# Kernel tuning notes

Measured on AMD Instinct MI355X. Metric: run time of the kernel, lower is better.

The kernel has to match this reference:

```python
import jax, jax.numpy as jnp
import numpy as np

D_MODEL = 1024
NUM_HEADS = 16
THETA = 10000.0


def setup_inputs() -> dict:
    key = jax.random.key(0)
    ks = jax.random.split(key, 5)
    B, S, D = 4, 2048, D_MODEL
    std = float(np.sqrt(2.0 / (D + D)))
    x = jax.random.normal(ks[0], (B, S, D), dtype=jnp.float32)
    wq = jax.random.normal(ks[1], (D, D), dtype=jnp.float32) * std
    wk = jax.random.normal(ks[2], (D, D), dtype=jnp.float32) * std
    wv = jax.random.normal(ks[3], (D, D), dtype=jnp.float32) * std
    wo = jax.random.normal(ks[4], (D, D), dtype=jnp.float32) * std
    token_positions = jnp.broadcast_to(jnp.arange(S, dtype=jnp.int32), (B, S))
    return {"x": x, "token_positions": token_positions,
            "wq": wq, "wk": wk, "wv": wv, "wo": wo}


def _rope(t, token_positions, d_k):
    # t: [B, H, S, d_k]; token_positions: [B, S]
    freqs = 1.0 / (THETA ** (jnp.arange(0, d_k, 2, dtype=jnp.float32) / d_k))  # [d_k/2]
    angles = token_positions.astype(jnp.float32)[..., None] * freqs            # [B, S, d_k/2]
    angles = jnp.repeat(angles, 2, axis=-1)                                    # [B, S, d_k]
    cos = jnp.cos(angles)[:, None, :, :]  # broadcast over heads
    sin = jnp.sin(angles)[:, None, :, :]
    t1, t2 = t[..., 0::2], t[..., 1::2]
    t_rot = jnp.stack([-t2, t1], axis=-1).reshape(t.shape)  # interleave (-x2, x1)
    return t * cos + t_rot * sin


def reference(x, token_positions, wq, wk, wv, wo):
    B, S, D = x.shape
    H = NUM_HEADS
    d_k = D // H
    def proj(w):
        return (x @ w.T).reshape(B, S, H, d_k).transpose(0, 2, 1, 3)  # [B,H,S,dk]
    q = _rope(proj(wq), token_positions, d_k)
    k = _rope(proj(wk), token_positions, d_k)
    v = proj(wv)
    scale = 1.0 / jnp.sqrt(jnp.float32(d_k))
    scores = jnp.einsum('bhqd,bhkd->bhqk', q, k) * scale  # [B,H,S,S]
    causal = jnp.tril(jnp.ones((S, S), dtype=bool))
    scores = jnp.where(causal, scores, -jnp.inf)
    attn = jax.nn.softmax(scores, axis=-1)
    out = jnp.einsum('bhqk,bhkd->bhqd', attn, v)          # [B,H,S,dk]
    out = out.transpose(0, 2, 1, 3).reshape(B, S, D)
    return out @ wo.T
```

## Files before the change

### kernel.cpp

```cpp
#include <hip/hip_runtime.h>
#include <hip/hip_bf16.h>
#include <cstdint>
#include <cstddef>

#define B_ 4
#define S_ 2048
#define D_ 1024
#define H_ 16
#define DK_ 64
#define NTOK (B_*S_)

typedef __bf16 bf16;
typedef __bf16 bf16x8 __attribute__((ext_vector_type(8)));
typedef short s16x4 __attribute__((ext_vector_type(4)));
typedef float f32x4 __attribute__((ext_vector_type(4)));

#define AS1 __attribute__((address_space(1)))
#define AS3 __attribute__((address_space(3)))

static __device__ __forceinline__ short f2bf_s(float f) {
    return __builtin_bit_cast(short, (__bf16)f);
}

static __device__ __forceinline__ f32x4 mfma16(s16x4 a, s16x4 b, f32x4 c) {
#if __has_builtin(__builtin_amdgcn_mfma_f32_16x16x16bf16_1k)
    return __builtin_amdgcn_mfma_f32_16x16x16bf16_1k(a, b, c, 0, 0, 0);
#else
    asm volatile("v_mfma_f32_16x16x16_bf16 %0, %1, %2, %0\n\ts_nop 7\n\ts_nop 7"
                 : "+v"(c) : "v"(a), "v"(b));
    return c;
#endif
}

__global__ void cvt_all(const float* __restrict__ x, const float* __restrict__ wq,
                        const float* __restrict__ wk, const float* __restrict__ wv,
                        const float* __restrict__ wo, bf16* __restrict__ dst) {
    const int NX8 = NTOK * D_ / 8;
    const int W8 = D_ * D_ / 8;
    int i = blockIdx.x * blockDim.x + threadIdx.x;
    if (i >= NX8 + 4 * W8) return;
    const float* src; int j;
    if (i < NX8) { src = x; j = i; }
    else {
        int k = i - NX8;
        int w = k >> 17;
        j = k & (W8 - 1);
        src = w == 0 ? wq : (w == 1 ? wk : (w == 2 ? wv : wo));
    }
    const float4* s4 = reinterpret_cast<const float4*>(src) + (size_t)j * 2;
    float4 a = s4[0], b = s4[1];
    bf16x8 o;
    o[0] = (bf16)a.x; o[1] = (bf16)a.y; o[2] = (bf16)a.z; o[3] = (bf16)a.w;
    o[4] = (bf16)b.x; o[5] = (bf16)b.y; o[6] = (bf16)b.z; o[7] = (bf16)b.w;
    reinterpret_cast<bf16x8*>(dst)[i] = o;
}

__global__ void rope_table(const int* __restrict__ pos, float2* __restrict__ tab) {
    int i = blockIdx.x * blockDim.x + threadIdx.x;
    if (i >= NTOK * 32) return;
    int n = i >> 5, p = i & 31;
    float pf = (float)pos[n];
    float freq = powf(10000.0f, -(float)p * (1.0f / 32.0f));
    float ang = pf * freq;
    float s, c;
    sincosf(ang, &s, &c);
    tab[i] = make_float2(c, s);
}

__global__ __launch_bounds__(256, 2)
void gemm_qkv(const bf16* __restrict__ A, const bf16* __restrict__ Bw,
              bf16* __restrict__ Qr, bf16* __restrict__ Kz, bf16* __restrict__ VT,
              const float2* __restrict__ tab) {
    const float SCL2E = 0.125f * 1.44269504088896340736f;
    constexpr int NKT = 16;
    __shared__ alignas(16) bf16 lds[2][(128 + 128) * 64];
    const int tid = threadIdx.x;
    const int lane = tid & 63;
    const int wid = tid >> 6;
    const int wm = wid >> 1, wn = wid & 1;
    const int lr = lane & 15, lg = lane >> 4;
    const int m0 = blockIdx.x * 128;
    const int n0g = blockIdx.y * 128;

    f32x4 acc[4][4] = {};

    auto stage = [&](int kt, int bufi) {
        bf16* dst = &lds[bufi][0];
#pragma unroll
        for (int j = 0; j < 4; ++j) {
            int flat = j * 256 + tid;
            int r = flat >> 3, c = flat & 7;
            const bf16* src = A + (size_t)(m0 + r) * 1024 + kt * 64 + ((c ^ (r & 7)) << 3);
            __builtin_amdgcn_global_load_lds((const AS1 uint32_t*)src,
                                             (AS3 uint32_t*)(dst + (size_t)flat * 8), 16, 0, 0);
        }
#pragma unroll
        for (int j = 0; j < 4; ++j) {
            int flat = j * 256 + tid;
            int r = flat >> 3, c = flat & 7;
            const bf16* src = Bw + (size_t)(n0g + r) * 1024 + kt * 64 + ((c ^ (r & 7)) << 3);
            __builtin_amdgcn_global_load_lds((const AS1 uint32_t*)src,
                                             (AS3 uint32_t*)(dst + 128 * 64 + (size_t)flat * 8), 16, 0, 0);
        }
    };

    stage(0, 0);

    for (int kt = 0; kt < NKT; ++kt) {
        const bf16* bufA = &lds[kt & 1][0];
        const bf16* bufB = bufA + 128 * 64;

        asm volatile("" ::: "memory");
        __builtin_amdgcn_s_barrier();
        asm volatile("" ::: "memory");
        if (kt + 1 < NKT) {
            stage(kt + 1, (kt + 1) & 1);
            asm volatile("s_waitcnt vmcnt(8)" ::: "memory");
        } else {
            asm volatile("s_waitcnt vmcnt(0)" ::: "memory");
        }
        __builtin_amdgcn_s_barrier();
        asm volatile("" ::: "memory");

        const int sx = lr & 7;
        bf16x8 af[4][2], bfr[4][2];
#pragma unroll
        for (int mf = 0; mf < 4; ++mf)
#pragma unroll
            for (int kh = 0; kh < 2; ++kh)
                af[mf][kh] = *reinterpret_cast<const bf16x8*>(
                    &bufA[(wm * 64 + mf * 16 + lr) * 64 + (((kh * 4 + lg) ^ sx) << 3)]);
#pragma unroll
        for (int nf = 0; nf < 4; ++nf)
#pragma unroll
            for (int kh = 0; kh < 2; ++kh)
                bfr[nf][kh] = *reinterpret_cast<const bf16x8*>(
                    &bufB[(wn * 64 + nf * 16 + lr) * 64 + (((kh * 4 + lg) ^ sx) << 3)]);
        __builtin_amdgcn_s_setprio(1);
#pragma unroll
        for (int mf = 0; mf < 4; ++mf)
#pragma unroll
            for (int nf = 0; nf < 4; ++nf)
#pragma unroll
                for (int kh = 0; kh < 2; ++kh)
                    acc[mf][nf] = __builtin_amdgcn_mfma_f32_16x16x32_bf16(af[mf][kh], bfr[nf][kh], acc[mf][nf], 0, 0, 0);
        __builtin_amdgcn_s_setprio(0);
    }

#pragma unroll
    for (int mf = 0; mf < 4; ++mf) {
#pragma unroll
        for (int nf = 0; nf < 4; ++nf) {
            int row0 = m0 + wm * 64 + mf * 16 + lg * 4;
            int colg = n0g + wn * 64 + nf * 16 + lr;
            int which = colg >> 10;
            int col = colg & 1023;
            if (which < 2) {
#pragma unroll
                for (int r = 0; r < 4; ++r) {
                    int row = row0 + r;
                    float v = acc[mf][nf][r];
                    float partner = __shfl_xor(v, 1, 64);
                    float2 cs = tab[(size_t)row * 32 + ((col >> 1) & 31)];
                    float o = (col & 1) ? fmaf(v, cs.x, partner * cs.y)
                                        : fmaf(v, cs.x, -partner * cs.y);
                    if (which == 0) {
                        Qr[(size_t)row * 1024 + col] = (bf16)(o * SCL2E);
                    } else {
                        int h = col >> 6, e = col & 63;
                        int e2 = e ^ ((row & 7) << 3);
                        Kz[(size_t)row * 1024 + h * 64 + e2] = (bf16)o;
                    }
                }
            } else {
                int h = col >> 6, dd = col & 63;
                int kvb = row0 & 63;
                int sw = (((dd & 7) ^ ((dd >> 3) & 7)) & 7) << 3;
                s16x4 pk;
#pragma unroll
                for (int r = 0; r < 4; ++r) pk[r] = f2bf_s(acc[mf][nf][r]);
                size_t addr = ((((size_t)((row0 >> 11) * 16 + h)) * 32 + ((row0 >> 6) & 31)) * 64 + dd) * 64
                              + (size_t)(kvb ^ sw);
                *reinterpret_cast<s16x4*>(&VT[addr]) = pk;
            }
        }
    }
}

__global__ __launch_bounds__(256, 2)
void gemm_out(const bf16* __restrict__ A, const bf16* __restrict__ Bw,
              float* __restrict__ Cp) {
    constexpr int NKT = 16;
    __shared__ alignas(16) bf16 lds[2][(128 + 128) * 64];
    const int tid = threadIdx.x;
    const int lane = tid & 63;
    const int wid = tid >> 6;
    const int wm = wid >> 1, wn = wid & 1;
    const int lr = lane & 15, lg = lane >> 4;
    const int m0 = blockIdx.x * 128;
    const int n0g = blockIdx.y * 128;

    f32x4 acc[4][4] = {};

    auto stage = [&](int kt, int bufi) {
        bf16* dst = &lds[bufi][0];
#pragma unroll
        for (int j = 0; j < 4; ++j) {
            int flat = j * 256 + tid;
            int r = flat >> 3, c = flat & 7;
            const bf16* src = A + (size_t)(m0 + r) * 1024 + kt * 64 + ((c ^ (r & 7)) << 3);
            __builtin_amdgcn_global_load_lds((const AS1 uint32_t*)src,
                                             (AS3 uint32_t*)(dst + (size_t)flat * 8), 16, 0, 0);
        }
#pragma unroll
        for (int j = 0; j < 4; ++j) {
            int flat = j * 256 + tid;
            int r = flat >> 3, c = flat & 7;
            const bf16* src = Bw + (size_t)(n0g + r) * 1024 + kt * 64 + ((c ^ (r & 7)) << 3);
            __builtin_amdgcn_global_load_lds((const AS1 uint32_t*)src,
                                             (AS3 uint32_t*)(dst + 128 * 64 + (size_t)flat * 8), 16, 0, 0);
        }
    };

    stage(0, 0);

    for (int kt = 0; kt < NKT; ++kt) {
        const bf16* bufA = &lds[kt & 1][0];
        const bf16* bufB = bufA + 128 * 64;

        asm volatile("" ::: "memory");
        __builtin_amdgcn_s_barrier();
        asm volatile("" ::: "memory");
        if (kt + 1 < NKT) {
            stage(kt + 1, (kt + 1) & 1);
            asm volatile("s_waitcnt vmcnt(8)" ::: "memory");
        } else {
            asm volatile("s_waitcnt vmcnt(0)" ::: "memory");
        }
        __builtin_amdgcn_s_barrier();
        asm volatile("" ::: "memory");

        const int sx = lr & 7;
        bf16x8 af[4][2], bfr[4][2];
#pragma unroll
        for (int mf = 0; mf < 4; ++mf)
#pragma unroll
            for (int kh = 0; kh < 2; ++kh)
                af[mf][kh] = *reinterpret_cast<const bf16x8*>(
                    &bufA[(wm * 64 + mf * 16 + lr) * 64 + (((kh * 4 + lg) ^ sx) << 3)]);
#pragma unroll
        for (int nf = 0; nf < 4; ++nf)
#pragma unroll
            for (int kh = 0; kh < 2; ++kh)
                bfr[nf][kh] = *reinterpret_cast<const bf16x8*>(
                    &bufB[(wn * 64 + nf * 16 + lr) * 64 + (((kh * 4 + lg) ^ sx) << 3)]);
        __builtin_amdgcn_s_setprio(1);
#pragma unroll
        for (int mf = 0; mf < 4; ++mf)
#pragma unroll
            for (int nf = 0; nf < 4; ++nf)
#pragma unroll
                for (int kh = 0; kh < 2; ++kh)
                    acc[mf][nf] = __builtin_amdgcn_mfma_f32_16x16x32_bf16(af[mf][kh], bfr[nf][kh], acc[mf][nf], 0, 0, 0);
        __builtin_amdgcn_s_setprio(0);
    }

#pragma unroll
    for (int mf = 0; mf < 4; ++mf)
#pragma unroll
        for (int nf = 0; nf < 4; ++nf)
#pragma unroll
            for (int r = 0; r < 4; ++r) {
                int row = m0 + wm * 64 + mf * 16 + lg * 4 + r;
                int colg = n0g + wn * 64 + nf * 16 + lr;
                Cp[(size_t)row * 1024 + colg] = acc[mf][nf][r];
            }
}

__global__ __launch_bounds__(256, 2)
void flash_attn9(const bf16* __restrict__ Q, const bf16* __restrict__ Kz,
                 const bf16* __restrict__ VT, bf16* __restrict__ O) {
    __shared__ bf16 Ks[2][64 * 64];
    __shared__ bf16 Vt[2][64 * 64];
    const int tid = threadIdx.x, lane = tid & 63, w = tid >> 6;
    const int lr = lane & 15, lg = lane >> 4;
    const int qtA = blockIdx.x;
    const int qtB = 15 - qtA;
    const int q0[2] = { qtA * 128, qtB * 128 };
    const int ntS[2] = { 2 * qtA + 2, 2 * qtB + 2 };
    const int NT = ntS[1];
    const int bh = blockIdx.y;
    const int b = bh >> 4, h = bh & 15;
    const size_t base = ((size_t)b * S_) * D_ + (size_t)h * DK_;
    const size_t vtbase = (size_t)bh * 32 * 4096;

    bf16x8 aq[2][2][2];
#pragma unroll
    for (int si = 0; si < 2; ++si)
#pragma unroll
        for (int qs = 0; qs < 2; ++qs) {
            int qrow = q0[si] + w * 32 + qs * 16 + lr;
            const bf16* qp = Q + base + (size_t)qrow * D_ + lg * 8;
            aq[si][qs][0] = *reinterpret_cast<const bf16x8*>(qp);
            aq[si][qs][1] = *reinterpret_cast<const bf16x8*>(qp + 32);
        }

    f32x4 acc[2][2][4] = {};
    float m_run[2][2] = {{-1e30f, -1e30f}, {-1e30f, -1e30f}};
    float l_run[2][2] = {{0.f, 0.f}, {0.f, 0.f}};

    const int sjj = tid >> 3;
    const int se0 = (tid & 7) * 8;

    auto stage = [&](int t, int bufi) {
        bf16* kd = Ks[bufi];
        bf16* vd = Vt[bufi];
#pragma unroll
        for (int i = 0; i < 2; ++i) {
            int jj = sjj + i * 32;
            const bf16* ksrc = Kz + base + (size_t)(t * 64 + jj) * 1024 + se0;
            __builtin_amdgcn_global_load_lds((const AS1 uint32_t*)ksrc,
                                             (AS3 uint32_t*)(kd + jj * 64 + se0), 16, 0, 0);
            const bf16* vsrc = VT + vtbase + (size_t)t * 4096 + jj * 64 + se0;
            __builtin_amdgcn_global_load_lds((const AS1 uint32_t*)vsrc,
                                             (AS3 uint32_t*)(vd + jj * 64 + se0), 16, 0, 0);
        }
    };

    stage(0, 0);

    for (int t = 0; t < NT; ++t) {
        const int j0 = t * 64;
        const bf16* KsB = Ks[t & 1];
        const bf16* VtB = Vt[t & 1];

        asm volatile("" ::: "memory");
        __builtin_amdgcn_s_barrier();
        asm volatile("" ::: "memory");
        if (t + 1 < NT) {
            stage(t + 1, (t + 1) & 1);
            asm volatile("s_waitcnt vmcnt(4)" ::: "memory");
        } else {
            asm volatile("s_waitcnt vmcnt(0)" ::: "memory");
        }
        __builtin_amdgcn_s_barrier();
        asm volatile("" ::: "memory");

#pragma unroll
        for (int si = 0; si < 2; ++si) {
            if (t >= ntS[si]) continue;
            const int qmaxw = q0[si] + w * 32 + 31;
            if (j0 > qmaxw) continue;

            f32x4 sc[2][4];
            __builtin_amdgcn_s_setprio(1);
#pragma unroll
            for (int nt = 0; nt < 4; ++nt) {
                int krow = nt * 16 + lr;
                int swz = (krow & 7) << 3;
                bf16x8 a0 = *reinterpret_cast<const bf16x8*>(&KsB[krow * 64 + ((lg * 8) ^ swz)]);
                bf16x8 a1 = *reinterpret_cast<const bf16x8*>(&KsB[krow * 64 + ((32 + lg * 8) ^ swz)]);
#pragma unroll
                for (int qs = 0; qs < 2; ++qs) {
                    f32x4 tv = {};
                    tv = __builtin_amdgcn_mfma_f32_16x16x32_bf16(a0, aq[si][qs][0], tv, 0, 0, 0);
                    tv = __builtin_amdgcn_mfma_f32_16x16x32_bf16(a1, aq[si][qs][1], tv, 0, 0, 0);
                    sc[qs][nt] = tv;
                }
            }
            __builtin_amdgcn_s_setprio(0);

            s16x4 ap[2][4];
#pragma unroll
            for (int qs = 0; qs < 2; ++qs) {
                const int qrow = q0[si] + w * 32 + qs * 16 + lr;
                if (j0 + 63 > q0[si] + w * 32 + qs * 16) {
#pragma unroll
                    for (int nt = 0; nt < 4; ++nt)
#pragma unroll
                        for (int r = 0; r < 4; ++r) {
                            int kv = j0 + nt * 16 + lg * 4 + r;
                            if (kv > qrow) sc[qs][nt][r] = -1e30f;
                        }
                }
                float tmax = sc[qs][0][0];
#pragma unroll
                for (int nt = 0; nt < 4; ++nt)
#pragma unroll
                    for (int r = 0; r < 4; ++r) tmax = fmaxf(tmax, sc[qs][nt][r]);
                tmax = fmaxf(tmax, __shfl_xor(tmax, 16, 64));
                tmax = fmaxf(tmax, __shfl_xor(tmax, 32, 64));
                float mold = m_run[si][qs];
                if (!__all(tmax - mold <= 8.0f)) {
                    float mnew = fmaxf(mold, tmax);
                    float corr = exp2f(mold - mnew);
                    m_run[si][qs] = mnew;
                    l_run[si][qs] *= corr;
#pragma unroll
                    for (int r = 0; r < 4; ++r) {
                        float cr = __shfl(corr, (lane & 48) | (lg * 4 + r), 64);
#pragma unroll
                        for (int dt = 0; dt < 4; ++dt) acc[si][qs][dt][r] *= cr;
                    }
                }
                float mnow = m_run[si][qs];
                float rs = 0.f;
#pragma unroll
                for (int nt = 0; nt < 4; ++nt)
#pragma unroll
                    for (int r = 0; r < 4; ++r) {
                        float p = exp2f(sc[qs][nt][r] - mnow);
                        rs += p;
                        ap[qs][nt][r] = f2bf_s(p);
                    }
                rs += __shfl_xor(rs, 16, 64);
                rs += __shfl_xor(rs, 32, 64);
                l_run[si][qs] += rs;
            }

            __builtin_amdgcn_s_setprio(1);
#pragma unroll
            for (int dt = 0; dt < 4; ++dt) {
                int vrow = dt * 16 + lr;
                int vswz = (((vrow & 7) ^ (vrow >> 3)) & 7) << 3;
                s16x4 bv[4];
#pragma unroll
                for (int nt = 0; nt < 4; ++nt)
                    bv[nt] = *reinterpret_cast<const s16x4*>(&VtB[vrow * 64 + ((nt * 16 + lg * 4) ^ vswz)]);
#pragma unroll
                for (int qs = 0; qs < 2; ++qs)
#pragma unroll
                    for (int nt = 0; nt < 4; ++nt)
                        acc[si][qs][dt] = mfma16(ap[qs][nt], bv[nt], acc[si][qs][dt]);
            }
            __builtin_amdgcn_s_setprio(0);
        }
    }

#pragma unroll
    for (int si = 0; si < 2; ++si)
#pragma unroll
        for (int qs = 0; qs < 2; ++qs) {
            float inv = __builtin_amdgcn_rcpf(l_run[si][qs]);
#pragma unroll
            for (int r = 0; r < 4; ++r) {
                float invr = __shfl(inv, (lane & 48) | (lg * 4 + r), 64);
                int row = q0[si] + w * 32 + qs * 16 + lg * 4 + r;
#pragma unroll
                for (int dt = 0; dt < 4; ++dt)
                    O[base + (size_t)row * D_ + dt * 16 + lr] = (bf16)(acc[si][qs][dt][r] * invr);
            }
        }
}

extern "C" void kernel_launch(void* const* d_in, const int* in_sizes, int n_in,
                              void* d_out, int out_size, void* d_ws, size_t ws_size,
                              hipStream_t stream) {
    const float* x  = (const float*)d_in[0];
    const int*   tp = (const int*)d_in[1];
    const float* wq = (const float*)d_in[2];
    const float* wk = (const float*)d_in[3];
    const float* wv = (const float*)d_in[4];
    const float* wo = (const float*)d_in[5];

    bf16* ws = (bf16*)d_ws;
    bf16* Xbf = ws;
    bf16* Wqb = Xbf + (size_t)NTOK * D_;
    bf16* Wkb = Wqb + (size_t)D_ * D_;
    bf16* Wvb = Wkb + (size_t)D_ * D_;
    bf16* Wob = Wvb + (size_t)D_ * D_;
    bf16* Qr  = Wob + (size_t)D_ * D_;
    bf16* Kz  = Qr + (size_t)NTOK * D_;
    bf16* VT  = Kz + (size_t)NTOK * D_;
    bf16* AO  = VT + (size_t)NTOK * D_;
    float2* tab = (float2*)(AO + (size_t)NTOK * D_);
    (void)ws_size; (void)in_sizes; (void)n_in; (void)out_size;
    (void)Wkb; (void)Wvb;

    {
        int ntot8 = (NTOK * D_ + 4 * D_ * D_) / 8;
        cvt_all<<<(ntot8 + 255) / 256, 256, 0, stream>>>(x, wq, wk, wv, wo, Xbf);
    }
    rope_table<<<(NTOK * 32 + 255) / 256, 256, 0, stream>>>(tp, tab);

    gemm_qkv<<<dim3(NTOK / 128, 24), 256, 0, stream>>>(Xbf, Wqb, Qr, Kz, VT, tab);

    flash_attn9<<<dim3(8, B_ * H_), 256, 0, stream>>>(Qr, Kz, VT, AO);

    gemm_out<<<dim3(NTOK / 128, D_ / 128), 256, 0, stream>>>(AO, Wob, (float*)d_out);
}
```

Before: 214.0 us.

## Split GEMM B-tile prefetch mid-iteration and batch attention score MFMAs across strips

Result: no change. 211.9 us (-1.0%).

```diff
diff --git a/kernel.cpp b/kernel.cpp
--- a/kernel.cpp
+++ b/kernel.cpp
@@ -84,7 +84,7 @@
 
     f32x4 acc[4][4] = {};
 
-    auto stage = [&](int kt, int bufi) {
+    auto stageA = [&](int kt, int bufi) {
         bf16* dst = &lds[bufi][0];
 #pragma unroll
         for (int j = 0; j < 4; ++j) {
@@ -94,17 +94,21 @@
             __builtin_amdgcn_global_load_lds((const AS1 uint32_t*)src,
                                              (AS3 uint32_t*)(dst + (size_t)flat * 8), 16, 0, 0);
         }
+    };
+    auto stageB = [&](int kt, int bufi) {
+        bf16* dst = &lds[bufi][0] + 128 * 64;
 #pragma unroll
         for (int j = 0; j < 4; ++j) {
             int flat = j * 256 + tid;
             int r = flat >> 3, c = flat & 7;
             const bf16* src = Bw + (size_t)(n0g + r) * 1024 + kt * 64 + ((c ^ (r & 7)) << 3);
             __builtin_amdgcn_global_load_lds((const AS1 uint32_t*)src,
-                                             (AS3 uint32_t*)(dst + 128 * 64 + (size_t)flat * 8), 16, 0, 0);
+                                             (AS3 uint32_t*)(dst + (size_t)flat * 8), 16, 0, 0);
         }
     };
 
-    stage(0, 0);
+    stageA(0, 0);
+    stageB(0, 0);
 
     for (int kt = 0; kt < NKT; ++kt) {
         const bf16* bufA = &lds[kt & 1][0];
@@ -114,8 +118,8 @@
         __builtin_amdgcn_s_barrier();
         asm volatile("" ::: "memory");
         if (kt + 1 < NKT) {
-            stage(kt + 1, (kt + 1) & 1);
-            asm volatile("s_waitcnt vmcnt(8)" ::: "memory");
+            stageA(kt + 1, (kt + 1) & 1);
+            asm volatile("s_waitcnt vmcnt(4)" ::: "memory");
         } else {
             asm volatile("s_waitcnt vmcnt(0)" ::: "memory");
         }
@@ -131,7 +135,7 @@
                 af[mf][kh] = *reinterpret_cast<const bf16x8*>(
                     &bufA[(wm * 64 + mf * 16 + lr) * 64 + (((kh * 4 + lg) ^ sx) << 3)]);
 #pragma unroll
-        for (int nf = 0; nf < 4; ++nf)
+        for (int nf = 0; nf < 2; ++nf)
 #pragma unroll
             for (int kh = 0; kh < 2; ++kh)
                 bfr[nf][kh] = *reinterpret_cast<const bf16x8*>(
@@ -140,7 +144,26 @@
 #pragma unroll
         for (int mf = 0; mf < 4; ++mf)
 #pragma unroll
-            for (int nf = 0; nf < 4; ++nf)
+            for (int nf = 0; nf < 2; ++nf)
+#pragma unroll
+                for (int kh = 0; kh < 2; ++kh)
+                    acc[mf][nf] = __builtin_amdgcn_mfma_f32_16x16x32_bf16(af[mf][kh], bfr[nf][kh], acc[mf][nf], 0, 0, 0);
+        __builtin_amdgcn_s_setprio(0);
+        if (kt + 1 < NKT) stageB(kt + 1, (kt + 1) & 1);
+        asm volatile("" ::: "memory");
+        __builtin_amdgcn_s_barrier();
+        asm volatile("" ::: "memory");
+#pragma unroll
+        for (int nf = 2; nf < 4; ++nf)
+#pragma unroll
+            for (int kh = 0; kh < 2; ++kh)
+                bfr[nf][kh] = *reinterpret_cast<const bf16x8*>(
+                    &bufB[(wn * 64 + nf * 16 + lr) * 64 + (((kh * 4 + lg) ^ sx) << 3)]);
+        __builtin_amdgcn_s_setprio(1);
+#pragma unroll
+        for (int mf = 0; mf < 4; ++mf)
+#pragma unroll
+            for (int nf = 2; nf < 4; ++nf)
 #pragma unroll
                 for (int kh = 0; kh < 2; ++kh)
                     acc[mf][nf] = __builtin_amdgcn_mfma_f32_16x16x32_bf16(af[mf][kh], bfr[nf][kh], acc[mf][nf], 0, 0, 0);
@@ -202,7 +225,7 @@
 
     f32x4 acc[4][4] = {};
 
-    auto stage = [&](int kt, int bufi) {
+    auto stageA = [&](int kt, int bufi) {
         bf16* dst = &lds[bufi][0];
 #pragma unroll
         for (int j = 0; j < 4; ++j) {
@@ -212,17 +235,21 @@
             __builtin_amdgcn_global_load_lds((const AS1 uint32_t*)src,
                                              (AS3 uint32_t*)(dst + (size_t)flat * 8), 16, 0, 0);
         }
+    };
+    auto stageB = [&](int kt, int bufi) {
+        bf16* dst = &lds[bufi][0] + 128 * 64;
 #pragma unroll
         for (int j = 0; j < 4; ++j) {
             int flat = j * 256 + tid;
             int r = flat >> 3, c = flat & 7;
             const bf16* src = Bw + (size_t)(n0g + r) * 1024 + kt * 64 + ((c ^ (r & 7)) << 3);
             __builtin_amdgcn_global_load_lds((const AS1 uint32_t*)src,
-                                             (AS3 uint32_t*)(dst + 128 * 64 + (size_t)flat * 8), 16, 0, 0);
+                                             (AS3 uint32_t*)(dst + (size_t)flat * 8), 16, 0, 0);
         }
     };
 
-    stage(0, 0);
+    stageA(0, 0);
+    stageB(0, 0);
 
     for (int kt = 0; kt < NKT; ++kt) {
         const bf16* bufA = &lds[kt & 1][0];
@@ -232,8 +259,8 @@
         __builtin_amdgcn_s_barrier();
         asm volatile("" ::: "memory");
         if (kt + 1 < NKT) {
-            stage(kt + 1, (kt + 1) & 1);
-            asm volatile("s_waitcnt vmcnt(8)" ::: "memory");
+            stageA(kt + 1, (kt + 1) & 1);
+            asm volatile("s_waitcnt vmcnt(4)" ::: "memory");
         } else {
             asm volatile("s_waitcnt vmcnt(0)" ::: "memory");
         }
@@ -249,7 +276,7 @@
                 af[mf][kh] = *reinterpret_cast<const bf16x8*>(
                     &bufA[(wm * 64 + mf * 16 + lr) * 64 + (((kh * 4 + lg) ^ sx) << 3)]);
 #pragma unroll
-        for (int nf = 0; nf < 4; ++nf)
+        for (int nf = 0; nf < 2; ++nf)
 #pragma unroll
             for (int kh = 0; kh < 2; ++kh)
                 bfr[nf][kh] = *reinterpret_cast<const bf16x8*>(
@@ -258,7 +285,26 @@
 #pragma unroll
         for (int mf = 0; mf < 4; ++mf)
 #pragma unroll
-            for (int nf = 0; nf < 4; ++nf)
+            for (int nf = 0; nf < 2; ++nf)
+#pragma unroll
+                for (int kh = 0; kh < 2; ++kh)
+                    acc[mf][nf] = __builtin_amdgcn_mfma_f32_16x16x32_bf16(af[mf][kh], bfr[nf][kh], acc[mf][nf], 0, 0, 0);
+        __builtin_amdgcn_s_setprio(0);
+        if (kt + 1 < NKT) stageB(kt + 1, (kt + 1) & 1);
+        asm volatile("" ::: "memory");
+        __builtin_amdgcn_s_barrier();
+        asm volatile("" ::: "memory");
+#pragma unroll
+        for (int nf = 2; nf < 4; ++nf)
+#pragma unroll
+            for (int kh = 0; kh < 2; ++kh)
+                bfr[nf][kh] = *reinterpret_cast<const bf16x8*>(
+                    &bufB[(wn * 64 + nf * 16 + lr) * 64 + (((kh * 4 + lg) ^ sx) << 3)]);
+        __builtin_amdgcn_s_setprio(1);
+#pragma unroll
+        for (int mf = 0; mf < 4; ++mf)
+#pragma unroll
+            for (int nf = 2; nf < 4; ++nf)
 #pragma unroll
                 for (int kh = 0; kh < 2; ++kh)
                     acc[mf][nf] = __builtin_amdgcn_mfma_f32_16x16x32_bf16(af[mf][kh], bfr[nf][kh], acc[mf][nf], 0, 0, 0);
@@ -278,8 +324,8 @@
 }
 
 __global__ __launch_bounds__(256, 2)
-void flash_attn9(const bf16* __restrict__ Q, const bf16* __restrict__ Kz,
-                 const bf16* __restrict__ VT, bf16* __restrict__ O) {
+void flash_attn10(const bf16* __restrict__ Q, const bf16* __restrict__ Kz,
+                  const bf16* __restrict__ VT, bf16* __restrict__ O) {
     __shared__ bf16 Ks[2][64 * 64];
     __shared__ bf16 Vt[2][64 * 64];
     const int tid = threadIdx.x, lane = tid & 63, w = tid >> 6;
@@ -346,14 +392,14 @@
         __builtin_amdgcn_s_barrier();
         asm volatile("" ::: "memory");
 
+        const bool act[2] = { t < ntS[0] && j0 <= q0[0] + w * 32 + 31,
+                              j0 <= q0[1] + w * 32 + 31 };
+        f32x4 sc[2][2][4];
+
+        __builtin_amdgcn_s_setprio(1);
 #pragma unroll
         for (int si = 0; si < 2; ++si) {
-            if (t >= ntS[si]) continue;
-            const int qmaxw = q0[si] + w * 32 + 31;
-            if (j0 > qmaxw) continue;
-
-            f32x4 sc[2][4];
-            __builtin_amdgcn_s_setprio(1);
+            if (!act[si]) continue;
 #pragma unroll
             for (int nt = 0; nt < 4; ++nt) {
                 int krow = nt * 16 + lr;
@@ -365,10 +411,15 @@
                     f32x4 tv = {};
                     tv = __builtin_amdgcn_mfma_f32_16x16x32_bf16(a0, aq[si][qs][0], tv, 0, 0, 0);
                     tv = __builtin_amdgcn_mfma_f32_16x16x32_bf16(a1, aq[si][qs][1], tv, 0, 0, 0);
-                    sc[qs][nt] = tv;
+                    sc[si][qs][nt] = tv;
                 }
             }
-            __builtin_amdgcn_s_setprio(0);
+        }
+        __builtin_amdgcn_s_setprio(0);
+
+#pragma unroll
+        for (int si = 0; si < 2; ++si) {
+            if (!act[si]) continue;
 
             s16x4 ap[2][4];
 #pragma unroll
@@ -380,14 +431,14 @@
 #pragma unroll
                         for (int r = 0; r < 4; ++r) {
                             int kv = j0 + nt * 16 + lg * 4 + r;
-                            if (kv > qrow) sc[qs][nt][r] = -1e30f;
+                            if (kv > qrow) sc[si][qs][nt][r] = -1e30f;
                         }
                 }
-                float tmax = sc[qs][0][0];
+                float tmax = sc[si][qs][0][0];
 #pragma unroll
                 for (int nt = 0; nt < 4; ++nt)
 #pragma unroll
-                    for (int r = 0; r < 4; ++r) tmax = fmaxf(tmax, sc[qs][nt][r]);
+                    for (int r = 0; r < 4; ++r) tmax = fmaxf(tmax, sc[si][qs][nt][r]);
                 tmax = fmaxf(tmax, __shfl_xor(tmax, 16, 64));
                 tmax = fmaxf(tmax, __shfl_xor(tmax, 32, 64));
                 float mold = m_run[si][qs];
@@ -409,7 +460,7 @@
                 for (int nt = 0; nt < 4; ++nt)
 #pragma unroll
                     for (int r = 0; r < 4; ++r) {
-                        float p = exp2f(sc[qs][nt][r] - mnow);
+                        float p = exp2f(sc[si][qs][nt][r] - mnow);
                         rs += p;
                         ap[qs][nt][r] = f2bf_s(p);
                     }
@@ -485,7 +536,7 @@
 
     gemm_qkv<<<dim3(NTOK / 128, 24), 256, 0, stream>>>(Xbf, Wqb, Qr, Kz, VT, tab);
 
-    flash_attn9<<<dim3(8, B_ * H_), 256, 0, stream>>>(Qr, Kz, VT, AO);
+    flash_attn10<<<dim3(8, B_ * H_), 256, 0, stream>>>(Qr, Kz, VT, AO);
 
     gemm_out<<<dim3(NTOK / 128, D_ / 128), 256, 0, stream>>>(AO, Wob, (float*)d_out);
 }
```
